# Performance work log

Hardware: AMD Instinct MI355X
Metric: run time of the kernel (lower is better)

## Reference

```python
import itertools
import jax, jax.numpy as jnp
import numpy as np

H, W, DIM, NH, WS = 64, 64, 384, 12, 7
HD = DIM // NH            # head dim = key_dim (attn_ratio=1)
N = WS * WS               # tokens per window
SCALE = HD ** -0.5
EPS = 1e-5
BATCH = 4
HID = int(DIM * 4.0)


def _bias_idxs():
    points = list(itertools.product(range(WS), range(WS)))
    offsets, idxs = {}, []
    for p1 in points:
        for p2 in points:
            off = (abs(p1[0] - p2[0]), abs(p1[1] - p2[1]))
            if off not in offsets:
                offsets[off] = len(offsets)
            idxs.append(offsets[off])
    return np.asarray(idxs, dtype=np.int32).reshape(N, N)

BIAS_IDXS = _bias_idxs()              # [N, N] static
NUM_OFFSETS = int(BIAS_IDXS.max()) + 1  # 49 for a 7x7 window


def setup_inputs() -> dict:
    key = jax.random.key(0)
    ks = jax.random.split(key, 10)
    rn = lambda k, shp, s=0.02: jax.random.normal(k, shp, jnp.float32) * s
    return {
        "x": jax.random.normal(ks[0], (BATCH, H * W, DIM), jnp.float32),
        "ln1_g": jnp.ones((DIM,), jnp.float32),
        "ln1_b": jnp.zeros((DIM,), jnp.float32),
        "qkv_w": rn(ks[1], (DIM, 3 * DIM)),
        "qkv_b": jnp.zeros((3 * DIM,), jnp.float32),
        "proj_w": rn(ks[2], (DIM, DIM)),
        "proj_b": jnp.zeros((DIM,), jnp.float32),
        "attn_bias": rn(ks[3], (NH, NUM_OFFSETS), 0.1),
        "conv_w": rn(ks[4], (DIM, 1, 3, 3), 0.1),  # depthwise OIHW
        "bn_g": jnp.ones((DIM,), jnp.float32),
        "bn_b": jnp.zeros((DIM,), jnp.float32),
        "bn_mean": rn(ks[5], (DIM,), 0.05),
        "bn_var": jax.random.uniform(ks[6], (DIM,), jnp.float32, 0.5, 1.5),
        "ln2_g": jnp.ones((DIM,), jnp.float32),
        "ln2_b": jnp.zeros((DIM,), jnp.float32),
        "fc1_w": rn(ks[7], (DIM, HID)),
        "fc1_b": jnp.zeros((HID,), jnp.float32),
        "fc2_w": rn(ks[8], (HID, DIM)),
        "fc2_b": jnp.zeros((DIM,), jnp.float32),
    }


def _ln(x, g, b):
    m = x.mean(-1, keepdims=True)
    v = jnp.var(x, axis=-1, keepdims=True)
    return (x - m) * jax.lax.rsqrt(v + EPS) * g + b


def reference(x, ln1_g, ln1_b, qkv_w, qkv_b, proj_w, proj_b, attn_bias,
              conv_w, bn_g, bn_b, bn_mean, bn_var, ln2_g, ln2_b,
              fc1_w, fc1_b, fc2_w, fc2_b):
    b, hw, c = x.shape
    res = x
    # --- window partition with padding ---
    pad_b = (-H) % WS
    pad_r = (-W) % WS
    pH, pW = H + pad_b, W + pad_r
    nH, nW = pH // WS, pW // WS
    xw = x.reshape(b, H, W, c)
    xw = jnp.pad(xw, ((0, 0), (0, pad_b), (0, pad_r), (0, 0)))
    xw = xw.reshape(b, nH, WS, nW, WS, c).transpose(0, 1, 3, 2, 4, 5)
    xw = xw.reshape(b * nH * nW, N, c)  # [Bw, N, C]
    # --- attention (pre-LN, relative position bias) ---
    xn = _ln(xw, ln1_g, ln1_b)
    qkv = (xn @ qkv_w + qkv_b).reshape(-1, N, NH, 3 * HD)
    q, k, v = jnp.split(qkv, [HD, 2 * HD], axis=-1)  # each [Bw, N, NH, HD]
    bias = attn_bias[:, BIAS_IDXS]                    # [NH, N, N]
    scores = jnp.einsum('bnhd,bmhd->bhnm', q, k) * SCALE + bias
    a = jax.nn.softmax(scores, axis=-1)
    o = jnp.einsum('bhnm,bmhd->bnhd', a, v).reshape(-1, N, NH * HD)
    xw = o @ proj_w + proj_b
    # --- window reverse + unpad ---
    xw = xw.reshape(b, nH, nW, WS, WS, c).transpose(0, 1, 3, 2, 4, 5)
    xw = xw.reshape(b, pH, pW, c)[:, :H, :W].reshape(b, hw, c)
    x = res + xw
    # --- depthwise 3x3 conv + BatchNorm (eval) ---
    xc = x.transpose(0, 2, 1).reshape(b, c, H, W)
    xc = jax.lax.conv_general_dilated(
        xc, conv_w, (1, 1), ((1, 1), (1, 1)),
        feature_group_count=c,
        dimension_numbers=('NCHW', 'OIHW', 'NCHW'))
    xc = (xc - bn_mean[:, None, None]) * jax.lax.rsqrt(bn_var[:, None, None] + EPS) \
         * bn_g[:, None, None] + bn_b[:, None, None]
    x = xc.reshape(b, c, hw).transpose(0, 2, 1)
    # --- MLP (pre-LN, GELU) with residual ---
    h1 = jax.nn.gelu(_ln(x, ln2_g, ln2_b) @ fc1_w + fc1_b, approximate=False)
    return x + (h1 @ fc2_w + fc2_b)
```

## Files before the change

### kernel.cpp

```cpp
#include <hip/hip_runtime.h>
#include <cstdint>


typedef __bf16 bf16x8 __attribute__((ext_vector_type(8)));
typedef __bf16 bf16x4 __attribute__((ext_vector_type(4)));
typedef float  f32x4  __attribute__((ext_vector_type(4)));

#define DIM_    384
#define QKVD    1152
#define HIDD    1536
#define NTOK    49
#define NWIN    400
#define MPAD    19712
#define MREAL   19600
#define TOKENS  16384
#define SCALE_  0.17677669529663689f
#define EPS_    1e-5f

__device__ __forceinline__ void gload_lds16(const void* g, void* l) {
  __builtin_amdgcn_global_load_lds(
      (__attribute__((address_space(1))) void*)g,
      (__attribute__((address_space(3))) void*)l, 16, 0, 0);
}

__device__ __forceinline__ float gelu_fast(float v) {
  float t2 = v * (1.5957691216057308f + 0.07135481627f * v * v);
  return v / (1.f + __expf(-t2));
}

__global__ void transpose_cast(const float* __restrict__ src, __bf16* __restrict__ dst,
                               int K, int N) {
  long id = (long)blockIdx.x * 256 + threadIdx.x;
  if (id >= (long)K * N) return;
  int  k = (int)(id % K);
  long n = id / K;
  dst[n * K + k] = (__bf16)src[(long)k * N + n];
}

__global__ void convw_transpose(const float* __restrict__ w, float* __restrict__ wT) {
  int id = blockIdx.x * 256 + threadIdx.x;
  if (id >= 3456) return;
  int ch = id / 9, k = id % 9;
  wT[k * 384 + ch] = w[id];
}

__global__ void bias_expand(const float* __restrict__ ab, float* __restrict__ bm) {
  int id = blockIdx.x * 256 + threadIdx.x;
  int h = id >> 12, q = (id >> 6) & 63, kk = id & 63;
  float v;
  if (kk >= NTOK)      v = -1e30f;
  else if (q >= NTOK)  v = 0.f;
  else {
    int idx = abs(q / 7 - kk / 7) * 7 + abs(q % 7 - kk % 7);
    v = ab[h * NTOK + idx];
  }
  bm[id] = v;
}

__global__ void ln1_window(const float* __restrict__ x, const float* __restrict__ gam,
                           const float* __restrict__ bet, __bf16* __restrict__ xn) {
  int t   = blockIdx.x;
  int tid = threadIdx.x;
  __bf16* orow = xn + (long)t * DIM_;
  if (t >= MREAL) {
    for (int i = tid; i < DIM_; i += 128) orow[i] = (__bf16)0.f;
    return;
  }
  int win = t / NTOK, tt = t % NTOK;
  int bb = win / 100, rem = win % 100;
  int r = (rem / 10) * 7 + tt / 7;
  int c = (rem % 10) * 7 + tt % 7;
  if (r >= 64 || c >= 64) {
    for (int i = tid; i < DIM_; i += 128) orow[i] = (__bf16)bet[i];
    return;
  }
  const float* xr = x + ((long)bb * 4096 + r * 64 + c) * DIM_;
  float v0 = xr[tid], v1 = xr[tid + 128], v2 = xr[tid + 256];
  float s = v0 + v1 + v2, s2 = v0 * v0 + v1 * v1 + v2 * v2;
  for (int off = 32; off; off >>= 1) { s += __shfl_down(s, off); s2 += __shfl_down(s2, off); }
  __shared__ float red[4];
  if ((tid & 63) == 0) { red[tid >> 6] = s; red[2 + (tid >> 6)] = s2; }
  __syncthreads();
  float S = red[0] + red[1], S2 = red[2] + red[3];
  float m  = S * (1.f / DIM_);
  float rs = rsqrtf(S2 * (1.f / DIM_) - m * m + EPS_);
  orow[tid]       = (__bf16)((v0 - m) * rs * gam[tid]       + bet[tid]);
  orow[tid + 128] = (__bf16)((v1 - m) * rs * gam[tid + 128] + bet[tid + 128]);
  orow[tid + 256] = (__bf16)((v2 - m) * rs * gam[tid + 256] + bet[tid + 256]);
}

__global__ __launch_bounds__(384) void conv_bn_ln2(
    const float* __restrict__ x1, const float* __restrict__ wT,
    const float* __restrict__ bng, const float* __restrict__ bnb,
    const float* __restrict__ mean, const float* __restrict__ var,
    const float* __restrict__ g2, const float* __restrict__ b2,
    float* __restrict__ x2, __bf16* __restrict__ xln2) {
  int tid = threadIdx.x;
  int p = tid / 96, g = tid % 96;
  int pix = blockIdx.x * 4 + p;
  int bb = pix >> 12, rc = pix & 4095;
  int r = rc >> 6, c = rc & 63;
  int ch = g << 2;

  f32x4 acc = (f32x4){0.f, 0.f, 0.f, 0.f};
  #pragma unroll
  for (int dr = -1; dr <= 1; dr++) {
    int rr = r + dr;
    if (rr < 0 || rr >= 64) continue;
    #pragma unroll
    for (int dc = -1; dc <= 1; dc++) {
      int cc = c + dc;
      if (cc < 0 || cc >= 64) continue;
      f32x4 xv = *(const f32x4*)(x1 + ((long)bb * 4096 + rr * 64 + cc) * DIM_ + ch);
      f32x4 wv = *(const f32x4*)(wT + ((dr + 1) * 3 + (dc + 1)) * DIM_ + ch);
      acc += xv * wv;
    }
  }

  f32x4 gv = *(const f32x4*)(bng + ch);
  f32x4 vv = *(const f32x4*)(var + ch);
  f32x4 mv = *(const f32x4*)(mean + ch);
  f32x4 bv = *(const f32x4*)(bnb + ch);
  f32x4 y;
  #pragma unroll
  for (int j = 0; j < 4; j++) {
    float sc = gv[j] * rsqrtf(vv[j] + EPS_);
    y[j] = acc[j] * sc + (bv[j] - mv[j] * sc);
  }
  *(f32x4*)(x2 + (long)pix * DIM_ + ch) = y;

  __shared__ float pS[4][96], pS2[4][96], mS[4], rS[4];
  pS[p][g]  = y[0] + y[1] + y[2] + y[3];
  pS2[p][g] = y[0] * y[0] + y[1] * y[1] + y[2] * y[2] + y[3] * y[3];
  __syncthreads();
  if (g < 32) {
    float a  = pS[p][g]  + pS[p][g + 32]  + pS[p][g + 64];
    float a2 = pS2[p][g] + pS2[p][g + 32] + pS2[p][g + 64];
    #pragma unroll
    for (int off = 1; off < 32; off <<= 1) {
      a  += __shfl_xor(a, off);
      a2 += __shfl_xor(a2, off);
    }
    if (g == 0) {
      float m = a * (1.f / DIM_);
      mS[p] = m;
      rS[p] = rsqrtf(a2 * (1.f / DIM_) - m * m + EPS_);
    }
  }
  __syncthreads();
  float m = mS[p], rs = rS[p];
  f32x4 gg = *(const f32x4*)(g2 + ch);
  f32x4 b2v = *(const f32x4*)(b2 + ch);
  bf16x4 ov;
  #pragma unroll
  for (int j = 0; j < 4; j++) ov[j] = (__bf16)((y[j] - m) * rs * gg[j] + b2v[j]);
  *(bf16x4*)(xln2 + (long)pix * DIM_ + ch) = ov;
}

__global__ __launch_bounds__(64) void attn_mfma(const __bf16* __restrict__ qkv,
                                                const float* __restrict__ bm,
                                                __bf16* __restrict__ o) {
  int blk = blockIdx.x;
  int win = blk / 12, h = blk % 12;
  int lane = threadIdx.x;
  int quad = lane >> 4, l16 = lane & 15;

  __shared__ __align__(16) __bf16 Vt[32][72];
  __shared__ __align__(16) __bf16 P[64][72];

  const __bf16* base = qkv + (long)win * NTOK * QKVD + h * 96;

  bf16x8 qf[4], kf[4];
  #pragma unroll
  for (int t = 0; t < 4; t++) {
    const __bf16* rp = base + (long)(t * 16 + l16) * QKVD + quad * 8;
    qf[t] = *(const bf16x8*)(rp);
    kf[t] = *(const bf16x8*)(rp + 32);
  }
  {
    const __bf16* vp = base + (long)lane * QKVD + 64;
    bf16x8 vv[4];
    #pragma unroll
    for (int i = 0; i < 4; i++) vv[i] = *(const bf16x8*)(vp + i * 8);
    #pragma unroll
    for (int i = 0; i < 4; i++)
      #pragma unroll
      for (int j = 0; j < 8; j++) Vt[i * 8 + j][lane] = vv[i][j];
  }

  f32x4 S[4][4];
  #pragma unroll
  for (int i = 0; i < 4; i++)
    #pragma unroll
    for (int j = 0; j < 4; j++) S[i][j] = (f32x4){0.f, 0.f, 0.f, 0.f};
  #pragma unroll
  for (int mt = 0; mt < 4; mt++)
    #pragma unroll
    for (int nt = 0; nt < 4; nt++)
      S[mt][nt] = __builtin_amdgcn_mfma_f32_16x16x32_bf16(qf[mt], kf[nt], S[mt][nt], 0, 0, 0);

  const float* bmh = bm + h * 4096;
  #pragma unroll
  for (int mt = 0; mt < 4; mt++)
    #pragma unroll
    for (int r = 0; r < 4; r++) {
      int q = mt * 16 + quad * 4 + r;
      #pragma unroll
      for (int nt = 0; nt < 4; nt++)
        S[mt][nt][r] = S[mt][nt][r] * SCALE_ + bmh[q * 64 + nt * 16 + l16];
    }

  #pragma unroll
  for (int mt = 0; mt < 4; mt++)
    #pragma unroll
    for (int r = 0; r < 4; r++) {
      float mx = fmaxf(fmaxf(S[mt][0][r], S[mt][1][r]), fmaxf(S[mt][2][r], S[mt][3][r]));
      #pragma unroll
      for (int off = 1; off < 16; off <<= 1) mx = fmaxf(mx, __shfl_xor(mx, off));
      float sum = 0.f;
      #pragma unroll
      for (int nt = 0; nt < 4; nt++) {
        float e = __expf(S[mt][nt][r] - mx);
        S[mt][nt][r] = e;
        sum += e;
      }
      #pragma unroll
      for (int off = 1; off < 16; off <<= 1) sum += __shfl_xor(sum, off);
      float inv = 1.f / sum;
      #pragma unroll
      for (int nt = 0; nt < 4; nt++) S[mt][nt][r] *= inv;
    }

  #pragma unroll
  for (int mt = 0; mt < 4; mt++)
    #pragma unroll
    for (int r = 0; r < 4; r++) {
      int q = mt * 16 + quad * 4 + r;
      #pragma unroll
      for (int nt = 0; nt < 4; nt++)
        P[q][nt * 16 + l16] = (__bf16)S[mt][nt][r];
    }
  __syncthreads();

  f32x4 O[4][2];
  #pragma unroll
  for (int i = 0; i < 4; i++)
    #pragma unroll
    for (int j = 0; j < 2; j++) O[i][j] = (f32x4){0.f, 0.f, 0.f, 0.f};
  #pragma unroll
  for (int kt = 0; kt < 2; kt++) {
    bf16x8 pf[4], vf[2];
    #pragma unroll
    for (int mt = 0; mt < 4; mt++)
      pf[mt] = *(const bf16x8*)(&P[mt * 16 + l16][kt * 32 + quad * 8]);
    #pragma unroll
    for (int nt = 0; nt < 2; nt++)
      vf[nt] = *(const bf16x8*)(&Vt[nt * 16 + l16][kt * 32 + quad * 8]);
    #pragma unroll
    for (int mt = 0; mt < 4; mt++)
      #pragma unroll
      for (int nt = 0; nt < 2; nt++)
        O[mt][nt] = __builtin_amdgcn_mfma_f32_16x16x32_bf16(pf[mt], vf[nt], O[mt][nt], 0, 0, 0);
  }

  __bf16* ob = o + (long)win * NTOK * DIM_ + h * 32;
  #pragma unroll
  for (int mt = 0; mt < 4; mt++)
    #pragma unroll
    for (int r = 0; r < 4; r++) {
      int q = mt * 16 + quad * 4 + r;
      if (q < NTOK) {
        #pragma unroll
        for (int nt = 0; nt < 2; nt++)
          ob[(long)q * DIM_ + nt * 16 + l16] = (__bf16)O[mt][nt][r];
      }
    }
}

template <int MODE, int TN>
__global__ void __launch_bounds__(256)
gemm_bf16(const __bf16* __restrict__ A, const __bf16* __restrict__ Bt,
          const float* __restrict__ bias, int K, int N,
          float* __restrict__ outf, __bf16* __restrict__ outb,
          const float* __restrict__ res) {
  constexpr int NT = TN / 32;
  __shared__ __align__(16) __bf16 sA[128 * 32];
  __shared__ __align__(16) __bf16 sB[TN * 32];
  int tid = threadIdx.x, lane = tid & 63, wid = tid >> 6;
  int wm = wid >> 1, wn = wid & 1;
  int quad = lane >> 4, l16 = lane & 15;
  long tileM = (long)blockIdx.x * 128;
  long tileN = (long)blockIdx.y * TN;

  f32x4 acc[4][NT];
  #pragma unroll
  for (int i = 0; i < 4; i++)
    #pragma unroll
    for (int j = 0; j < NT; j++) acc[i][j] = (f32x4){0.f, 0.f, 0.f, 0.f};

  int rr = wid * 16 + (lane >> 2);
  const __bf16* gA = A  + (tileM + rr) * (long)K + ((lane & 3) << 3);
  const __bf16* gB = Bt + (tileN + rr) * (long)K + ((lane & 3) << 3);
  const long rowskip = 64 * (long)K;

  for (int k0 = 0; k0 < K; k0 += 32) {
    gload_lds16(gA + k0,           sA + (wid << 9));
    gload_lds16(gA + k0 + rowskip, sA + ((wid + 4) << 9));
    gload_lds16(gB + k0,           sB + (wid << 9));
    if (TN == 128)
      gload_lds16(gB + k0 + rowskip, sB + ((wid + 4) << 9));
    __syncthreads();
    bf16x8 af[4], bfr[NT];
    #pragma unroll
    for (int mt = 0; mt < 4; mt++)
      af[mt] = *(const bf16x8*)(sA + ((wm * 64 + mt * 16 + l16) << 5) + (quad << 3));
    #pragma unroll
    for (int nt = 0; nt < NT; nt++)
      bfr[nt] = *(const bf16x8*)(sB + ((wn * (TN / 2) + nt * 16 + l16) << 5) + (quad << 3));
    #pragma unroll
    for (int mt = 0; mt < 4; mt++)
      #pragma unroll
      for (int nt = 0; nt < NT; nt++)
        acc[mt][nt] = __builtin_amdgcn_mfma_f32_16x16x32_bf16(af[mt], bfr[nt], acc[mt][nt], 0, 0, 0);
    __syncthreads();
  }

  float bcol[NT];
  #pragma unroll
  for (int nt = 0; nt < NT; nt++) bcol[nt] = bias[tileN + wn * (TN / 2) + nt * 16 + l16];

  #pragma unroll
  for (int mt = 0; mt < 4; mt++) {
    #pragma unroll
    for (int r = 0; r < 4; r++) {
      long row = tileM + wm * 64 + mt * 16 + quad * 4 + r;
      if (MODE == 0) {
        __bf16* orow = outb + row * (long)N;
        #pragma unroll
        for (int nt = 0; nt < NT; nt++)
          orow[tileN + wn * (TN / 2) + nt * 16 + l16] = (__bf16)(acc[mt][nt][r] + bcol[nt]);
      } else if (MODE == 1) {
        if (row < MREAL) {
          int r32 = (int)row;
          int win = r32 / NTOK, t = r32 % NTOK;
          int rem = win % 100;
          int pr = (rem / 10) * 7 + t / 7;
          int pc = (rem % 10) * 7 + t % 7;
          if (pr < 64 && pc < 64) {
            long po = ((long)(win / 100) * 4096 + pr * 64 + pc) * DIM_;
            #pragma unroll
            for (int nt = 0; nt < NT; nt++) {
              long col = tileN + wn * (TN / 2) + nt * 16 + l16;
              outf[po + col] = res[po + col] + acc[mt][nt][r] + bcol[nt];
            }
          }
        }
      } else if (MODE == 2) {
        __bf16* orow = outb + row * (long)N;
        #pragma unroll
        for (int nt = 0; nt < NT; nt++) {
          float v = acc[mt][nt][r] + bcol[nt];
          orow[tileN + wn * (TN / 2) + nt * 16 + l16] = (__bf16)gelu_fast(v);
        }
      } else {
        float* orow = outf + row * (long)N;
        const float* rrow = res + row * (long)N;
        #pragma unroll
        for (int nt = 0; nt < NT; nt++) {
          long col = tileN + wn * (TN / 2) + nt * 16 + l16;
          orow[col] = acc[mt][nt][r] + bcol[nt] + rrow[col];
        }
      }
    }
  }
}

extern "C" void kernel_launch(void* const* d_in, const int* in_sizes, int n_in,
                              void* d_out, int out_size, void* d_ws, size_t ws_size,
                              hipStream_t stream) {
  const float* x       = (const float*)d_in[0];
  const float* ln1_g   = (const float*)d_in[1];
  const float* ln1_b   = (const float*)d_in[2];
  const float* qkv_w   = (const float*)d_in[3];
  const float* qkv_b   = (const float*)d_in[4];
  const float* proj_w  = (const float*)d_in[5];
  const float* proj_b  = (const float*)d_in[6];
  const float* attn_b  = (const float*)d_in[7];
  const float* conv_w  = (const float*)d_in[8];
  const float* bn_g    = (const float*)d_in[9];
  const float* bn_b    = (const float*)d_in[10];
  const float* bn_mean = (const float*)d_in[11];
  const float* bn_var  = (const float*)d_in[12];
  const float* ln2_g   = (const float*)d_in[13];
  const float* ln2_b   = (const float*)d_in[14];
  const float* fc1_w   = (const float*)d_in[15];
  const float* fc1_b   = (const float*)d_in[16];
  const float* fc2_w   = (const float*)d_in[17];
  const float* fc2_b   = (const float*)d_in[18];

  char* p = (char*)d_ws;
  __bf16* WQKV = (__bf16*)p;  p += 884736;
  __bf16* WPROJ = (__bf16*)p; p += 294912;
  __bf16* WFC1 = (__bf16*)p;  p += 1179648;
  __bf16* WFC2 = (__bf16*)p;  p += 1179648;
  float*  WCONV = (float*)p;  p += 13824;
  char* region = p;           p += 75694080;
  float* X1 = (float*)p;      p += 25165824;
  float* X2 = (float*)p;      p += 25165824;
  __bf16* XN   = (__bf16*)region;
  float*  BM   = (float*)region;
  __bf16* QKVB = (__bf16*)(region + 15138816);
  __bf16* OBUF = (__bf16*)(region + 60555264);
  __bf16* XLN2 = (__bf16*)region;
  __bf16* H1   = (__bf16*)(region + 15138816);
  float* OUT = (float*)d_out;

  transpose_cast<<<(442368 + 255) / 256, 256, 0, stream>>>(qkv_w, WQKV, DIM_, QKVD);
  transpose_cast<<<(147456 + 255) / 256, 256, 0, stream>>>(proj_w, WPROJ, DIM_, DIM_);
  transpose_cast<<<(589824 + 255) / 256, 256, 0, stream>>>(fc1_w, WFC1, DIM_, HIDD);
  transpose_cast<<<(589824 + 255) / 256, 256, 0, stream>>>(fc2_w, WFC2, HIDD, DIM_);
  convw_transpose<<<14, 256, 0, stream>>>(conv_w, WCONV);

  ln1_window<<<MPAD, 128, 0, stream>>>(x, ln1_g, ln1_b, XN);

  gemm_bf16<0, 128><<<dim3(MPAD / 128, QKVD / 128), 256, 0, stream>>>(
      XN, WQKV, qkv_b, DIM_, QKVD, nullptr, QKVB, nullptr);

  bias_expand<<<192, 256, 0, stream>>>(attn_b, BM);

  attn_mfma<<<NWIN * 12, 64, 0, stream>>>(QKVB, BM, OBUF);

  gemm_bf16<1, 64><<<dim3(MPAD / 128, DIM_ / 64), 256, 0, stream>>>(
      OBUF, WPROJ, proj_b, DIM_, DIM_, X1, nullptr, x);

  conv_bn_ln2<<<TOKENS / 4, 384, 0, stream>>>(X1, WCONV, bn_g, bn_b, bn_mean, bn_var,
                                              ln2_g, ln2_b, X2, XLN2);

  gemm_bf16<2, 128><<<dim3(TOKENS / 128, HIDD / 128), 256, 0, stream>>>(
      XLN2, WFC1, fc1_b, DIM_, HIDD, nullptr, H1, nullptr);

  gemm_bf16<3, 64><<<dim3(TOKENS / 128, DIM_ / 64), 256, 0, stream>>>(
      H1, WFC2, fc2_b, HIDD, DIM_, OUT, nullptr, X2);
}
```

Before: 325.5 us.

## Fuse prep kernels into one launch and stage two K-slices per GEMM barrier

Merges the weight transposes, conv weight transpose, bias expansion and LN1 windowing into a single prep kernel dispatched by block range, removing several launches. The bias table moves into the X1 buffer so it can be written alongside XN. The GEMM main loop now loads two 32-wide K slices per sync, halving barriers at the cost of doubled LDS. GELU uses a hardware reciprocal instead of a division.

```diff
diff --git a/kernel.cpp b/kernel.cpp
--- a/kernel.cpp
+++ b/kernel.cpp
@@ -17,6 +17,15 @@
 #define SCALE_  0.17677669529663689f
 #define EPS_    1e-5f
 
+#define B_LN1   9856
+#define B_QKV   1728
+#define B_PROJ  576
+#define B_FC1   2304
+#define B_FC2   2304
+#define B_CONV  14
+#define B_BIAS  192
+#define B_TOTAL (B_LN1 + B_QKV + B_PROJ + B_FC1 + B_FC2 + B_CONV + B_BIAS)
+
 __device__ __forceinline__ void gload_lds16(const void* g, void* l) {
   __builtin_amdgcn_global_load_lds(
       (__attribute__((address_space(1))) void*)g,
@@ -25,68 +34,112 @@
 
 __device__ __forceinline__ float gelu_fast(float v) {
   float t2 = v * (1.5957691216057308f + 0.07135481627f * v * v);
-  return v / (1.f + __expf(-t2));
-}
-
-__global__ void transpose_cast(const float* __restrict__ src, __bf16* __restrict__ dst,
-                               int K, int N) {
-  long id = (long)blockIdx.x * 256 + threadIdx.x;
-  if (id >= (long)K * N) return;
-  int  k = (int)(id % K);
-  long n = id / K;
-  dst[n * K + k] = (__bf16)src[(long)k * N + n];
-}
-
-__global__ void convw_transpose(const float* __restrict__ w, float* __restrict__ wT) {
-  int id = blockIdx.x * 256 + threadIdx.x;
-  if (id >= 3456) return;
-  int ch = id / 9, k = id % 9;
-  wT[k * 384 + ch] = w[id];
-}
-
-__global__ void bias_expand(const float* __restrict__ ab, float* __restrict__ bm) {
-  int id = blockIdx.x * 256 + threadIdx.x;
-  int h = id >> 12, q = (id >> 6) & 63, kk = id & 63;
-  float v;
-  if (kk >= NTOK)      v = -1e30f;
-  else if (q >= NTOK)  v = 0.f;
-  else {
-    int idx = abs(q / 7 - kk / 7) * 7 + abs(q % 7 - kk % 7);
-    v = ab[h * NTOK + idx];
-  }
-  bm[id] = v;
-}
-
-__global__ void ln1_window(const float* __restrict__ x, const float* __restrict__ gam,
-                           const float* __restrict__ bet, __bf16* __restrict__ xn) {
-  int t   = blockIdx.x;
+  return v * __builtin_amdgcn_rcpf(1.f + __expf(-t2));
+}
+
+__global__ __launch_bounds__(256) void prep_all(
+    const float* __restrict__ x, const float* __restrict__ ln1_g,
+    const float* __restrict__ ln1_b, __bf16* __restrict__ xn,
+    const float* __restrict__ qkv_w,  __bf16* __restrict__ wqkv,
+    const float* __restrict__ proj_w, __bf16* __restrict__ wproj,
+    const float* __restrict__ fc1_w,  __bf16* __restrict__ wfc1,
+    const float* __restrict__ fc2_w,  __bf16* __restrict__ wfc2,
+    const float* __restrict__ conv_w, float* __restrict__ wconv,
+    const float* __restrict__ attn_b, float* __restrict__ bm) {
+  int b = blockIdx.x;
   int tid = threadIdx.x;
-  __bf16* orow = xn + (long)t * DIM_;
-  if (t >= MREAL) {
-    for (int i = tid; i < DIM_; i += 128) orow[i] = (__bf16)0.f;
-    return;
-  }
-  int win = t / NTOK, tt = t % NTOK;
-  int bb = win / 100, rem = win % 100;
-  int r = (rem / 10) * 7 + tt / 7;
-  int c = (rem % 10) * 7 + tt % 7;
-  if (r >= 64 || c >= 64) {
-    for (int i = tid; i < DIM_; i += 128) orow[i] = (__bf16)bet[i];
-    return;
-  }
-  const float* xr = x + ((long)bb * 4096 + r * 64 + c) * DIM_;
-  float v0 = xr[tid], v1 = xr[tid + 128], v2 = xr[tid + 256];
-  float s = v0 + v1 + v2, s2 = v0 * v0 + v1 * v1 + v2 * v2;
-  for (int off = 32; off; off >>= 1) { s += __shfl_down(s, off); s2 += __shfl_down(s2, off); }
-  __shared__ float red[4];
-  if ((tid & 63) == 0) { red[tid >> 6] = s; red[2 + (tid >> 6)] = s2; }
-  __syncthreads();
-  float S = red[0] + red[1], S2 = red[2] + red[3];
-  float m  = S * (1.f / DIM_);
-  float rs = rsqrtf(S2 * (1.f / DIM_) - m * m + EPS_);
-  orow[tid]       = (__bf16)((v0 - m) * rs * gam[tid]       + bet[tid]);
-  orow[tid + 128] = (__bf16)((v1 - m) * rs * gam[tid + 128] + bet[tid + 128]);
-  orow[tid + 256] = (__bf16)((v2 - m) * rs * gam[tid + 256] + bet[tid + 256]);
+
+  if (b < B_LN1) {
+    int sub = tid >> 7, tl = tid & 127;
+    int t = b * 2 + sub;
+    __bf16* orow = xn + (long)t * DIM_;
+    int kind;
+    int bb = 0, r = 0, c = 0;
+    if (t >= MREAL) kind = 2;
+    else {
+      int win = t / NTOK, tt = t % NTOK;
+      bb = win / 100;
+      int rem = win % 100;
+      r = (rem / 10) * 7 + tt / 7;
+      c = (rem % 10) * 7 + tt % 7;
+      kind = (r >= 64 || c >= 64) ? 1 : 0;
+    }
+    float v0 = 0.f, v1 = 0.f, v2 = 0.f;
+    if (kind == 0) {
+      const float* xr = x + ((long)bb * 4096 + r * 64 + c) * DIM_;
+      v0 = xr[tl]; v1 = xr[tl + 128]; v2 = xr[tl + 256];
+    }
+    float s = v0 + v1 + v2, s2 = v0 * v0 + v1 * v1 + v2 * v2;
+    for (int off = 32; off; off >>= 1) { s += __shfl_down(s, off); s2 += __shfl_down(s2, off); }
+    __shared__ float red[2][4];
+    if ((tl & 63) == 0) { red[sub][tl >> 6] = s; red[sub][2 + (tl >> 6)] = s2; }
+    __syncthreads();
+    float S = red[sub][0] + red[sub][1], S2 = red[sub][2] + red[sub][3];
+    float m  = S * (1.f / DIM_);
+    float rs = rsqrtf(S2 * (1.f / DIM_) - m * m + EPS_);
+    if (kind == 0) {
+      orow[tl]       = (__bf16)((v0 - m) * rs * ln1_g[tl]       + ln1_b[tl]);
+      orow[tl + 128] = (__bf16)((v1 - m) * rs * ln1_g[tl + 128] + ln1_b[tl + 128]);
+      orow[tl + 256] = (__bf16)((v2 - m) * rs * ln1_g[tl + 256] + ln1_b[tl + 256]);
+    } else if (kind == 1) {
+      orow[tl]       = (__bf16)ln1_b[tl];
+      orow[tl + 128] = (__bf16)ln1_b[tl + 128];
+      orow[tl + 256] = (__bf16)ln1_b[tl + 256];
+    } else {
+      orow[tl] = (__bf16)0.f; orow[tl + 128] = (__bf16)0.f; orow[tl + 256] = (__bf16)0.f;
+    }
+    return;
+  }
+  b -= B_LN1;
+  if (b < B_QKV) {
+    int id = b * 256 + tid;
+    int k = id % DIM_; int n = id / DIM_;
+    wqkv[id] = (__bf16)qkv_w[(long)k * QKVD + n];
+    return;
+  }
+  b -= B_QKV;
+  if (b < B_PROJ) {
+    int id = b * 256 + tid;
+    int k = id % DIM_; int n = id / DIM_;
+    wproj[id] = (__bf16)proj_w[(long)k * DIM_ + n];
+    return;
+  }
+  b -= B_PROJ;
+  if (b < B_FC1) {
+    int id = b * 256 + tid;
+    int k = id % DIM_; int n = id / DIM_;
+    wfc1[id] = (__bf16)fc1_w[(long)k * HIDD + n];
+    return;
+  }
+  b -= B_FC1;
+  if (b < B_FC2) {
+    int id = b * 256 + tid;
+    int k = id % HIDD; int n = id / HIDD;
+    wfc2[id] = (__bf16)fc2_w[(long)k * DIM_ + n];
+    return;
+  }
+  b -= B_FC2;
+  if (b < B_CONV) {
+    int id = b * 256 + tid;
+    if (id < 3456) {
+      int ch = id / 9, k = id % 9;
+      wconv[k * DIM_ + ch] = conv_w[id];
+    }
+    return;
+  }
+  b -= B_CONV;
+  {
+    int id = b * 256 + tid;
+    int h = id >> 12, q = (id >> 6) & 63, kk = id & 63;
+    float v;
+    if (kk >= NTOK)      v = -1e30f;
+    else if (q >= NTOK)  v = 0.f;
+    else {
+      int idx = abs(q / 7 - kk / 7) * 7 + abs(q % 7 - kk % 7);
+      v = attn_b[h * NTOK + idx];
+    }
+    bm[id] = v;
+  }
 }
 
 __global__ __launch_bounds__(384) void conv_bn_ln2(
@@ -284,8 +337,8 @@
           float* __restrict__ outf, __bf16* __restrict__ outb,
           const float* __restrict__ res) {
   constexpr int NT = TN / 32;
-  __shared__ __align__(16) __bf16 sA[128 * 32];
-  __shared__ __align__(16) __bf16 sB[TN * 32];
+  __shared__ __align__(16) __bf16 sA[2][128 * 32];
+  __shared__ __align__(16) __bf16 sB[2][TN * 32];
   int tid = threadIdx.x, lane = tid & 63, wid = tid >> 6;
   int wm = wid >> 1, wn = wid & 1;
   int quad = lane >> 4, l16 = lane & 15;
@@ -303,25 +356,32 @@
   const __bf16* gB = Bt + (tileN + rr) * (long)K + ((lane & 3) << 3);
   const long rowskip = 64 * (long)K;
 
-  for (int k0 = 0; k0 < K; k0 += 32) {
-    gload_lds16(gA + k0,           sA + (wid << 9));
-    gload_lds16(gA + k0 + rowskip, sA + ((wid + 4) << 9));
-    gload_lds16(gB + k0,           sB + (wid << 9));
-    if (TN == 128)
-      gload_lds16(gB + k0 + rowskip, sB + ((wid + 4) << 9));
+  for (int k0 = 0; k0 < K; k0 += 64) {
+    #pragma unroll
+    for (int h = 0; h < 2; h++) {
+      const int ko = k0 + h * 32;
+      gload_lds16(gA + ko,           &sA[h][wid << 9]);
+      gload_lds16(gA + ko + rowskip, &sA[h][(wid + 4) << 9]);
+      gload_lds16(gB + ko,           &sB[h][wid << 9]);
+      if (TN == 128)
+        gload_lds16(gB + ko + rowskip, &sB[h][(wid + 4) << 9]);
+    }
     __syncthreads();
-    bf16x8 af[4], bfr[NT];
-    #pragma unroll
-    for (int mt = 0; mt < 4; mt++)
-      af[mt] = *(const bf16x8*)(sA + ((wm * 64 + mt * 16 + l16) << 5) + (quad << 3));
-    #pragma unroll
-    for (int nt = 0; nt < NT; nt++)
-      bfr[nt] = *(const bf16x8*)(sB + ((wn * (TN / 2) + nt * 16 + l16) << 5) + (quad << 3));
-    #pragma unroll
-    for (int mt = 0; mt < 4; mt++)
+    #pragma unroll
+    for (int h = 0; h < 2; h++) {
+      bf16x8 af[4], bfr[NT];
+      #pragma unroll
+      for (int mt = 0; mt < 4; mt++)
+        af[mt] = *(const bf16x8*)(&sA[h][((wm * 64 + mt * 16 + l16) << 5) + (quad << 3)]);
       #pragma unroll
       for (int nt = 0; nt < NT; nt++)
-        acc[mt][nt] = __builtin_amdgcn_mfma_f32_16x16x32_bf16(af[mt], bfr[nt], acc[mt][nt], 0, 0, 0);
+        bfr[nt] = *(const bf16x8*)(&sB[h][((wn * (TN / 2) + nt * 16 + l16) << 5) + (quad << 3)]);
+      #pragma unroll
+      for (int mt = 0; mt < 4; mt++)
+        #pragma unroll
+        for (int nt = 0; nt < NT; nt++)
+          acc[mt][nt] = __builtin_amdgcn_mfma_f32_16x16x32_bf16(af[mt], bfr[nt], acc[mt][nt], 0, 0, 0);
+    }
     __syncthreads();
   }
 
@@ -408,26 +468,21 @@
   float* X1 = (float*)p;      p += 25165824;
   float* X2 = (float*)p;      p += 25165824;
   __bf16* XN   = (__bf16*)region;
-  float*  BM   = (float*)region;
   __bf16* QKVB = (__bf16*)(region + 15138816);
   __bf16* OBUF = (__bf16*)(region + 60555264);
   __bf16* XLN2 = (__bf16*)region;
   __bf16* H1   = (__bf16*)(region + 15138816);
+  float*  BM   = X1;
   float* OUT = (float*)d_out;
 
-  transpose_cast<<<(442368 + 255) / 256, 256, 0, stream>>>(qkv_w, WQKV, DIM_, QKVD);
-  transpose_cast<<<(147456 + 255) / 256, 256, 0, stream>>>(proj_w, WPROJ, DIM_, DIM_);
-  transpose_cast<<<(589824 + 255) / 256, 256, 0, stream>>>(fc1_w, WFC1, DIM_, HIDD);
-  transpose_cast<<<(589824 + 255) / 256, 256, 0, stream>>>(fc2_w, WFC2, HIDD, DIM_);
-  convw_transpose<<<14, 256, 0, stream>>>(conv_w, WCONV);
-
-  ln1_window<<<MPAD, 128, 0, stream>>>(x, ln1_g, ln1_b, XN);
+  prep_all<<<B_TOTAL, 256, 0, stream>>>(x, ln1_g, ln1_b, XN,
+                                        qkv_w, WQKV, proj_w, WPROJ,
+                                        fc1_w, WFC1, fc2_w, WFC2,
+                                        conv_w, WCONV, attn_b, BM);
 
   gemm_bf16<0, 128><<<dim3(MPAD / 128, QKVD / 128), 256, 0, stream>>>(
       XN, WQKV, qkv_b, DIM_, QKVD, nullptr, QKVB, nullptr);
 
-  bias_expand<<<192, 256, 0, stream>>>(attn_b, BM);
-
   attn_mfma<<<NWIN * 12, 64, 0, stream>>>(QKVB, BM, OBUF);
 
   gemm_bf16<1, 64><<<dim3(MPAD / 128, DIM_ / 64), 256, 0, stream>>>(
```

Result: faster. 296.7 us (-8.9%).
